# Kernel tuning notes

Hardware: AMD Instinct MI355X
Metric: run time of the kernel (lower is better)

The kernel has to match this reference:

```python
import jax, jax.numpy as jnp
import numpy as np

D_MODEL = 1024
N_HEAD = 16
D_QKV = 64
B, L = 2, 2048
LN_EPS = 1e-5


def setup_inputs() -> dict:
    key = jax.random.key(0)
    ks = jax.random.split(key, 5)
    # xavier-normal-ish scale for [H, d_model, d_qkv] params
    std_in = (2.0 / (D_MODEL + D_QKV)) ** 0.5
    return {
        "x": jax.random.normal(ks[0], (B, L, D_MODEL), jnp.float32),
        "w_q": jax.random.normal(ks[1], (N_HEAD, D_MODEL, D_QKV), jnp.float32) * std_in,
        "w_k": jax.random.normal(ks[2], (N_HEAD, D_MODEL, D_QKV), jnp.float32) * std_in,
        "w_v": jax.random.normal(ks[3], (N_HEAD, D_MODEL, D_QKV), jnp.float32) * std_in,
        "w_o": jax.random.normal(ks[4], (N_HEAD, D_QKV, D_MODEL), jnp.float32) * std_in,
        "ln_gamma": jnp.ones((D_MODEL,), jnp.float32),
        "ln_beta": jnp.zeros((D_MODEL,), jnp.float32),
    }


def reference(x, w_q, w_k, w_v, w_o, ln_gamma, ln_beta):
    # q,k,v: [B, H, L, d_qkv]
    q = jnp.einsum('hmq,blm->bhlq', w_q, x)
    k = jnp.einsum('hmq,blm->bhlq', w_k, x)
    v = jnp.einsum('hmq,blm->bhlq', w_v, x)
    # scores: [B, H, L, L]
    s = jnp.einsum('bhiq,bhjq->bhij', q, k) / (D_QKV ** 0.5)
    s = jax.nn.softmax(s, axis=-1)
    # (dropout disabled: eval-mode reference)
    att = jnp.einsum('bhij,bhjq->bhiq', s, v)          # [B, H, L, d_qkv]
    out = jnp.einsum('bhlq,hqm->blm', att, w_o)        # [B, L, d_model]
    y = x + out                                        # residual
    mu = jnp.mean(y, axis=-1, keepdims=True)
    var = jnp.var(y, axis=-1, keepdims=True)
    return (y - mu) * jax.lax.rsqrt(var + LN_EPS) * ln_gamma + ln_beta
```

## Files before the change

kernel.cpp:

```cpp
#include <hip/hip_runtime.h>
#include <hip/hip_bf16.h>
#include <cstdint>

#define B_      2
#define L_      2048
#define DM_     1024
#define H_      16
#define DQ_     64
#define LN_EPS  1e-5f
#define QSCALE  0.1803368801111204f

typedef unsigned short u16;
typedef unsigned int   u32;
typedef __attribute__((ext_vector_type(8)))  short short8;
typedef __attribute__((ext_vector_type(4)))  unsigned short u16x4;
typedef __attribute__((ext_vector_type(4)))  unsigned int   u32x4;
typedef __attribute__((ext_vector_type(4)))  float f32x4;
typedef __attribute__((ext_vector_type(16))) float f32x16;

__device__ __forceinline__ u16 f2b(float f) {
  __hip_bfloat16 h = __float2bfloat16(f);
  return *reinterpret_cast<u16*>(&h);
}
__device__ __forceinline__ u32 pk2(float lo, float hi) {
  return (u32)f2b(lo) | ((u32)f2b(hi) << 16);
}

__device__ __forceinline__ void gl_lds16(const void* g, void* l) {
  auto gp = reinterpret_cast<const __attribute__((address_space(1))) unsigned int*>(
      reinterpret_cast<uintptr_t>(g));
  auto lp = reinterpret_cast<__attribute__((address_space(3))) unsigned int*>(
      reinterpret_cast<uintptr_t>(l));
  __builtin_amdgcn_global_load_lds(gp, lp, 16, 0, 0);
}

__device__ __forceinline__ void bar() { asm volatile("s_barrier" ::: "memory"); }

__device__ __forceinline__ short8 frag8(const u16* base, int row, int lchunk) {
  return *(const short8*)(base + row * 64 + ((lchunk ^ (row & 7)) << 3));
}

__global__ __launch_bounds__(256) void prep_all(
    const float* __restrict__ x, const float* __restrict__ wq,
    const float* __restrict__ wk, const float* __restrict__ wv,
    const float* __restrict__ wo, u16* __restrict__ xb,
    u16* __restrict__ wt, u16* __restrict__ wot) {
  __shared__ float Ls[64][65];
  const int t = threadIdx.x;
  const int bx = blockIdx.x;
  if (bx < 4096) {
    int i = bx * 256 + t;
    float4 v = ((const float4*)x)[i];
    u16x4 o = { f2b(v.x), f2b(v.y), f2b(v.z), f2b(v.w) };
    *(u16x4*)(xb + (size_t)i * 4) = o;
  } else if (bx < 4096 + 768) {
    int b2 = bx - 4096;
    int mt = b2 & 15, h = (b2 >> 4) & 15, wh = b2 >> 8;
    const float* in = ((wh == 0) ? wq : (wh == 1) ? wk : wv) + (size_t)h * DM_ * DQ_;
    #pragma unroll
    for (int i = 0; i < 16; ++i) {
      int idx = i * 256 + t, r = idx >> 6, c = idx & 63;
      Ls[r][c] = in[(size_t)(mt * 64 + r) * DQ_ + c];
    }
    __syncthreads();
    u16* outb = wt + (size_t)(wh * H_ + h) * DQ_ * DM_;
    #pragma unroll
    for (int i = 0; i < 16; ++i) {
      int idx = i * 256 + t, q = idx >> 6, mm = idx & 63;
      outb[(size_t)q * DM_ + mt * 64 + mm] = f2b(Ls[mm][q]);
    }
  } else {
    int b3 = bx - 4864;
    int mt = b3 & 15, kt = b3 >> 4;
    #pragma unroll
    for (int i = 0; i < 16; ++i) {
      int idx = i * 256 + t, r = idx >> 6, c = idx & 63;
      Ls[r][c] = wo[(size_t)(kt * 64 + r) * DM_ + mt * 64 + c];
    }
    __syncthreads();
    #pragma unroll
    for (int i = 0; i < 16; ++i) {
      int idx = i * 256 + t, mm = idx >> 6, kk = idx & 63;
      wot[(size_t)(mt * 64 + mm) * DM_ + kt * 64 + kk] = f2b(Ls[kk][mm]);
    }
  }
}

__global__ __launch_bounds__(512) void qkv_big(const u16* __restrict__ xb,
    const u16* __restrict__ wt, u16* __restrict__ Q, u16* __restrict__ K,
    u16* __restrict__ Vtg) {
  const int raw = blockIdx.x;
  const int swz = (raw & 7) * 24 + (raw >> 3);
  const int nt = swz >> 4, mt = swz & 15;
  __shared__ __align__(16) u16 SH[65536];
  u16* const A0 = SH;
  u16* const B0 = SH + 16384;
  u16* const A1 = SH + 32768;
  u16* const B1 = SH + 49152;
  const int t = threadIdx.x, w = t >> 6, lane = t & 63;
  const int lx = lane & 15, lq = lane >> 4;
  const int r8 = lane >> 3, lc = (lane & 7) ^ r8;
  const int row0 = mt * 256, n0 = nt * 256;
  const int wr = (w >> 2) * 128, wc = (w & 3) * 64;

  const u16* gA = xb + (size_t)(row0 + w * 32 + r8) * DM_ + lc * 8;
  const u16* gB = wt + (size_t)(n0  + w * 32 + r8) * DM_ + lc * 8;
  const int lw = (w * 32) * 64;

  #pragma unroll
  for (int s = 0; s < 4; ++s)
    gl_lds16(gA + (size_t)s * 8 * DM_, A0 + lw + s * 8 * 64);
  #pragma unroll
  for (int s = 0; s < 4; ++s)
    gl_lds16(gB + (size_t)s * 8 * DM_, B0 + lw + s * 8 * 64);
  gl_lds16(gA + 64 + (size_t)0 * 8 * DM_, A1 + lw + 0 * 8 * 64);
  gl_lds16(gA + 64 + (size_t)1 * 8 * DM_, A1 + lw + 1 * 8 * 64);
  asm volatile("s_waitcnt vmcnt(2)" ::: "memory");
  bar();

  f32x4 z = {0.f, 0.f, 0.f, 0.f};
  f32x4 acc[8][4];
  #pragma unroll
  for (int mf = 0; mf < 8; ++mf)
    #pragma unroll
    for (int nf = 0; nf < 4; ++nf) acc[mf][nf] = z;

  for (int tau = 0; tau < 16; ++tau) {
    const int d = tau & 1;
    u16* Ad = d ? A1 : A0;
    u16* Bd = d ? B1 : B0;
    u16* Ao = d ? A0 : A1;
    u16* Bo = d ? B0 : B1;
    const int t1 = (tau + 1 < 16) ? tau + 1 : 15;

    short8 af[8], bf[4];
    #pragma unroll
    for (int mf = 0; mf < 8; ++mf) af[mf] = frag8(Ad, wr + mf * 16 + lx, lq);
    #pragma unroll
    for (int nf = 0; nf < 4; ++nf) bf[nf] = frag8(Bd, wc + nf * 16 + lx, lq);

    gl_lds16(gA + (size_t)t1 * 64 + (size_t)2 * 8 * DM_, Ao + lw + 2 * 8 * 64);
    gl_lds16(gA + (size_t)t1 * 64 + (size_t)3 * 8 * DM_, Ao + lw + 3 * 8 * 64);
    #pragma unroll
    for (int s = 0; s < 4; ++s)
      gl_lds16(gB + (size_t)t1 * 64 + (size_t)s * 8 * DM_, Bo + lw + s * 8 * 64);

    #pragma unroll
    for (int nf = 0; nf < 4; ++nf)
      #pragma unroll
      for (int mf = 0; mf < 8; ++mf)
        acc[mf][nf] = __builtin_amdgcn_mfma_f32_16x16x32_bf16(af[mf], bf[nf], acc[mf][nf], 0, 0, 0);

    #pragma unroll
    for (int mf = 0; mf < 8; ++mf) af[mf] = frag8(Ad, wr + mf * 16 + lx, 4 | lq);
    #pragma unroll
    for (int nf = 0; nf < 4; ++nf) bf[nf] = frag8(Bd, wc + nf * 16 + lx, 4 | lq);
    #pragma unroll
    for (int nf = 0; nf < 4; ++nf)
      #pragma unroll
      for (int mf = 0; mf < 8; ++mf)
        acc[mf][nf] = __builtin_amdgcn_mfma_f32_16x16x32_bf16(af[mf], bf[nf], acc[mf][nf], 0, 0, 0);

    bar();

    const int t2 = (tau + 2 < 16) ? tau + 2 : 15;
    gl_lds16(gA + (size_t)t2 * 64 + (size_t)0 * 8 * DM_, Ad + lw + 0 * 8 * 64);
    gl_lds16(gA + (size_t)t2 * 64 + (size_t)1 * 8 * DM_, Ad + lw + 1 * 8 * 64);

    asm volatile("s_waitcnt vmcnt(2)" ::: "memory");
    bar();
  }
  asm volatile("s_waitcnt vmcnt(0)" ::: "memory");
  bar();

  const int wh  = nt >> 2;
  const float oscale = (wh == 0) ? QSCALE : 1.0f;
  const int bb  = row0 >> 11, l0 = row0 & 2047;
  const int hd0 = (nt & 3) * 256;
  u16* Ep = SH;

  if (wh != 2) {
    u16* outp = (wh == 0) ? Q : K;
    #pragma unroll
    for (int mp = 0; mp < 2; ++mp) {
      if ((w >> 2) == mp) {
        #pragma unroll
        for (int mf = 0; mf < 8; ++mf)
          #pragma unroll
          for (int nf = 0; nf < 4; ++nf)
            #pragma unroll
            for (int r = 0; r < 4; ++r) {
              int l = mf * 16 + lq * 4 + r;
              Ep[l * 264 + wc + nf * 16 + lx] = f2b(acc[mf][nf][r] * oscale);
            }
      }
      __syncthreads();
      #pragma unroll
      for (int hs = 0; hs < 4; ++hs) {
        const int hh = (hd0 >> 6) + hs;
        u16* gbase = outp + ((size_t)(bb * H_ + hh) * L_ + l0 + mp * 128) * DQ_;
        #pragma unroll
        for (int it = 0; it < 2; ++it) {
          int u = it * 512 + t;
          int l = u >> 3, ch = u & 7;
          *(uint4*)(gbase + (size_t)u * 8) = *(const uint4*)&Ep[l * 264 + hs * 64 + ch * 8];
        }
      }
      __syncthreads();
    }
  } else {
    #pragma unroll
    for (int mp = 0; mp < 2; ++mp) {
      if ((w >> 2) == mp) {
        #pragma unroll
        for (int mf = 0; mf < 8; ++mf)
          #pragma unroll
          for (int nf = 0; nf < 4; ++nf) {
            int ll = mf * 16 + lq * 4;
            int lp = (ll & ~12) | ((ll & 4) << 1) | ((ll & 8) >> 1);
            int dd = wc + nf * 16 + lx;
            uint2 pv = { pk2(acc[mf][nf][0], acc[mf][nf][1]),
                         pk2(acc[mf][nf][2], acc[mf][nf][3]) };
            *(uint2*)&Ep[dd * 136 + lp] = pv;
          }
      }
      __syncthreads();
      #pragma unroll
      for (int it = 0; it < 8; ++it) {
        int v = it * 512 + t;
        int dloc = v >> 4, ch = v & 15;
        int hh = (hd0 + dloc) >> 6, ddg = (hd0 + dloc) & 63;
        u16* g = Vtg + ((size_t)(bb * H_ + hh) * DQ_ + ddg) * L_ + l0 + mp * 128 + ch * 8;
        *(uint4*)g = *(const uint4*)&Ep[dloc * 136 + ch * 8];
      }
      __syncthreads();
    }
  }
}

__global__ __launch_bounds__(512) void attn_mfma(const u16* __restrict__ Q,
    const u16* __restrict__ K, const u16* __restrict__ Vtg, u16* __restrict__ att) {
  const int ord = blockIdx.x;
  const int r_  = ord & 7, s_ = ord >> 3;
  const int qt  = s_ & 7, ghi = s_ >> 3;
  const int grp = r_ + 8 * ghi;
  const int h   = grp & 15, b = grp >> 4;
  __shared__ __align__(16) u16 Qs_[256 * 64];
  __shared__ __align__(16) u16 Ks_[2][64 * 64];
  __shared__ __align__(16) u16 Vt_[2][64 * 64];
  const int t = threadIdx.x, w = t >> 6, lane = t & 63;
  const int c = lane & 31, lsel = lane >> 5;
  const int r8 = lane >> 3, lc = (lane & 7) ^ r8;
  const size_t bh  = (size_t)(b * H_ + h) * L_ * DQ_;
  const size_t bhv = (size_t)(b * H_ + h) * DQ_ * L_;

  const u16* gQ = Q + bh + (size_t)(qt * 256 + w * 32 + r8) * DQ_ + lc * 8;
  #pragma unroll
  for (int i = 0; i < 4; ++i) gl_lds16(gQ + (size_t)i * 8 * DQ_, Qs_ + (w * 32 + i * 8) * 64);

  const u16* gK = K   + bh  + (size_t)(w * 8 + r8) * DQ_ + lc * 8;
  const u16* gV = Vtg + bhv + (size_t)(w * 8 + r8) * L_  + lc * 8;

  gl_lds16(gK, Ks_[0] + w * 8 * 64);
  gl_lds16(gV, Vt_[0] + w * 8 * 64);
  __syncthreads();
  short8 qb[4];
  #pragma unroll
  for (int km = 0; km < 4; ++km) qb[km] = frag8(Qs_, w * 32 + c, (km << 1) | lsel);

  f32x16 zz = {0.f,0.f,0.f,0.f,0.f,0.f,0.f,0.f,0.f,0.f,0.f,0.f,0.f,0.f,0.f,0.f};
  f32x16 oacc0 = zz, oacc1 = zz, lacc = zz;
  const short one_bf = (short)0x3F80;
  short8 ones = {one_bf, one_bf, one_bf, one_bf, one_bf, one_bf, one_bf, one_bf};

  for (int kt = 0; kt < L_ / 64; ++kt) {
    const int cur = kt & 1;
    __syncthreads();

    if (kt + 1 < L_ / 64) {
      const int nxt = 1 - cur;
      gl_lds16(gK + (size_t)(kt + 1) * 64 * DQ_, Ks_[nxt] + w * 8 * 64);
      gl_lds16(gV + (size_t)(kt + 1) * 64,       Vt_[nxt] + w * 8 * 64);
    }

    u32x4 paw[4];
    #pragma unroll
    for (int kb = 0; kb < 2; ++kb) {
      f32x16 s = zz;
      #pragma unroll
      for (int km = 0; km < 4; ++km) {
        short8 ka = frag8(Ks_[cur], kb * 32 + c, (km << 1) | lsel);
        s = __builtin_amdgcn_mfma_f32_32x32x16_bf16(ka, qb[km], s, 0, 0, 0);
      }
      #pragma unroll
      for (int F = 0; F < 2; ++F) {
        u32x4 pw;
        #pragma unroll
        for (int i = 0; i < 4; ++i) {
          float p0 = __builtin_amdgcn_exp2f(s[8 * F + 2 * i]);
          float p1 = __builtin_amdgcn_exp2f(s[8 * F + 2 * i + 1]);
          pw[i] = __builtin_amdgcn_perm(__float_as_uint(p1), __float_as_uint(p0), 0x07060302u);
        }
        paw[2 * kb + F] = pw;
      }
    }

    #pragma unroll
    for (int km = 0; km < 4; ++km) {
      short8 pa  = *reinterpret_cast<const short8*>(&paw[km]);
      short8 vb0 = frag8(Vt_[cur], c,      (km << 1) | lsel);
      short8 vb1 = frag8(Vt_[cur], 32 + c, (km << 1) | lsel);
      oacc0 = __builtin_amdgcn_mfma_f32_32x32x16_bf16(pa, vb0, oacc0, 0, 0, 0);
      oacc1 = __builtin_amdgcn_mfma_f32_32x32x16_bf16(pa, vb1, oacc1, 0, 0, 0);
      lacc  = __builtin_amdgcn_mfma_f32_32x32x16_bf16(pa, ones, lacc, 0, 0, 0);
    }
  }

  const int qrow_base = qt * 256 + w * 32;
  #pragma unroll
  for (int r = 0; r < 16; ++r) {
    int qr = (r & 3) + 8 * (r >> 2) + 4 * lsel;
    float inv = 1.0f / lacc[r];
    size_t base = (size_t)(b * L_ + qrow_base + qr) * DM_ + h * DQ_;
    att[base + c]      = f2b(oacc0[r] * inv);
    att[base + 32 + c] = f2b(oacc1[r] * inv);
  }
}

__global__ __launch_bounds__(256) void oproj_big(const u16* __restrict__ A,
    const u16* __restrict__ wot, float* __restrict__ out) {
  const int nt = blockIdx.x, mt = blockIdx.y;
  __shared__ __align__(16) u16 As_[128 * 64];
  __shared__ __align__(16) u16 Bs_[128 * 64];
  const int t = threadIdx.x, w = t >> 6, lane = t & 63;
  const int lx = lane & 15, lq = lane >> 4;
  const int row0 = mt * 128, n0 = nt * 128;
  const int r8 = lane >> 3, lc = (lane & 7) ^ r8;
  const int wr = (w >> 1) * 64, wc = (w & 1) * 64;

  const u16* gA = A   + (size_t)(row0 + w * 32 + r8) * DM_ + lc * 8;
  const u16* gB = wot + (size_t)(n0  + w * 32 + r8) * DM_ + lc * 8;
  u16* lA = As_ + (w * 32) * 64;
  u16* lB = Bs_ + (w * 32) * 64;

  f32x4 z = {0.f, 0.f, 0.f, 0.f};
  f32x4 acc[4][4];
  #pragma unroll
  for (int mb = 0; mb < 4; ++mb)
    #pragma unroll
    for (int nb = 0; nb < 4; ++nb) acc[mb][nb] = z;

  for (int k0 = 0; k0 < DM_; k0 += 64) {
    #pragma unroll
    for (int i = 0; i < 4; ++i) {
      gl_lds16(gA + (size_t)i * 8 * DM_ + k0, lA + i * 8 * 64);
      gl_lds16(gB + (size_t)i * 8 * DM_ + k0, lB + i * 8 * 64);
    }
    __syncthreads();
    short8 af[4][2];
    #pragma unroll
    for (int mb = 0; mb < 4; ++mb)
      #pragma unroll
      for (int kh = 0; kh < 2; ++kh)
        af[mb][kh] = frag8(As_, wr + mb * 16 + lx, (kh << 2) | lq);
    #pragma unroll
    for (int nb = 0; nb < 4; ++nb) {
      short8 b0 = frag8(Bs_, wc + nb * 16 + lx, lq);
      short8 b1 = frag8(Bs_, wc + nb * 16 + lx, 4 | lq);
      #pragma unroll
      for (int mb = 0; mb < 4; ++mb) {
        acc[mb][nb] = __builtin_amdgcn_mfma_f32_16x16x32_bf16(af[mb][0], b0, acc[mb][nb], 0, 0, 0);
        acc[mb][nb] = __builtin_amdgcn_mfma_f32_16x16x32_bf16(af[mb][1], b1, acc[mb][nb], 0, 0, 0);
      }
    }
    __syncthreads();
  }
  #pragma unroll
  for (int mb = 0; mb < 4; ++mb)
    #pragma unroll
    for (int nb = 0; nb < 4; ++nb)
      #pragma unroll
      for (int r = 0; r < 4; ++r) {
        int row = row0 + wr + mb * 16 + lq * 4 + r;
        out[(size_t)row * DM_ + n0 + wc + nb * 16 + lx] = acc[mb][nb][r];
      }
}

__global__ __launch_bounds__(256) void resid_ln(
    const float* __restrict__ x, const float* __restrict__ gamma,
    const float* __restrict__ beta, float* __restrict__ out) {
  const int row = blockIdx.x;
  const int t   = threadIdx.x;
  const float4* xp = (const float4*)(x   + (size_t)row * DM_);
  float4*       yp = (float4*)      (out + (size_t)row * DM_);

  float4 xv = xp[t];
  float4 av = yp[t];
  float y0 = xv.x + av.x, y1 = xv.y + av.y, y2 = xv.z + av.z, y3 = xv.w + av.w;

  float s  = y0 + y1 + y2 + y3;
  float s2 = y0 * y0 + y1 * y1 + y2 * y2 + y3 * y3;
  #pragma unroll
  for (int off = 32; off > 0; off >>= 1) {
    s  += __shfl_xor(s,  off, 64);
    s2 += __shfl_xor(s2, off, 64);
  }
  __shared__ float red[8];
  const int wave = t >> 6, lane = t & 63;
  if (lane == 0) { red[wave] = s; red[4 + wave] = s2; }
  __syncthreads();
  s  = red[0] + red[1] + red[2] + red[3];
  s2 = red[4] + red[5] + red[6] + red[7];

  const float mean = s * (1.f / DM_);
  const float var  = s2 * (1.f / DM_) - mean * mean;
  const float inv  = rsqrtf(var + LN_EPS);

  const float4 g  = ((const float4*)gamma)[t];
  const float4 bt = ((const float4*)beta)[t];
  float4 r;
  r.x = (y0 - mean) * inv * g.x + bt.x;
  r.y = (y1 - mean) * inv * g.y + bt.y;
  r.z = (y2 - mean) * inv * g.z + bt.z;
  r.w = (y3 - mean) * inv * g.w + bt.w;
  yp[t] = r;
}

extern "C" void kernel_launch(void* const* d_in, const int* in_sizes, int n_in,
                              void* d_out, int out_size, void* d_ws, size_t ws_size,
                              hipStream_t stream) {
  const float* x     = (const float*)d_in[0];
  const float* wq    = (const float*)d_in[1];
  const float* wk    = (const float*)d_in[2];
  const float* wv    = (const float*)d_in[3];
  const float* wo    = (const float*)d_in[4];
  const float* gamma = (const float*)d_in[5];
  const float* beta  = (const float*)d_in[6];
  float* out = (float*)d_out;

  char* ws = (char*)d_ws;
  u16* xb  = (u16*)ws;
  u16* Qb  = (u16*)(ws + ((size_t)8  << 20));
  u16* Kb  = (u16*)(ws + ((size_t)16 << 20));
  u16* Vtg = (u16*)(ws + ((size_t)24 << 20));
  u16* wt  = (u16*)(ws + ((size_t)32 << 20));
  u16* wot = (u16*)(ws + ((size_t)38 << 20));
  u16* att = (u16*)(ws + ((size_t)40 << 20));

  prep_all <<<5120, 256, 0, stream>>>(x, wq, wk, wv, wo, xb, wt, wot);
  qkv_big  <<<192, 512, 0, stream>>>(xb, wt, Qb, Kb, Vtg);
  attn_mfma<<<256, 512, 0, stream>>>(Qb, Kb, Vtg, att);
  oproj_big<<<dim3(8, 32), 256, 0, stream>>>(att, wot, out);
  resid_ln <<<B_ * L_, 256, 0, stream>>>(x, gamma, beta, out);
}
```

Measured before the change: 184.1 us.

## Split attention over two key halves and add a combine kernel

The attention kernel now splits the key/value sequence in two, launching twice as many blocks. Each block writes unnormalized fp32 partial outputs and row sums to workspace. A new attn_combine kernel adds the two partials, normalizes them and writes the bf16 attention output for the output projection. The aim is more blocks in flight per CU to hide latency in the attention loop. The cost is an extra launch and roughly tens of MB of fp32 partial traffic, and the workspace must hold buffers up to about 100 MB.

```diff
diff --git a/kernel.cpp b/kernel.cpp
--- a/kernel.cpp
+++ b/kernel.cpp
@@ -239,10 +239,11 @@
 }
 
 __global__ __launch_bounds__(512) void attn_mfma(const u16* __restrict__ Q,
-    const u16* __restrict__ K, const u16* __restrict__ Vtg, u16* __restrict__ att) {
+    const u16* __restrict__ K, const u16* __restrict__ Vtg,
+    float* __restrict__ Opart, float* __restrict__ lsum) {
   const int ord = blockIdx.x;
   const int r_  = ord & 7, s_ = ord >> 3;
-  const int qt  = s_ & 7, ghi = s_ >> 3;
+  const int qt  = s_ & 7, hf = (s_ >> 3) & 1, ghi = s_ >> 4;
   const int grp = r_ + 8 * ghi;
   const int h   = grp & 15, b = grp >> 4;
   __shared__ __align__(16) u16 Qs_[256 * 64];
@@ -253,13 +254,14 @@
   const int r8 = lane >> 3, lc = (lane & 7) ^ r8;
   const size_t bh  = (size_t)(b * H_ + h) * L_ * DQ_;
   const size_t bhv = (size_t)(b * H_ + h) * DQ_ * L_;
+  const int kb0 = hf * (L_ / 2);
 
   const u16* gQ = Q + bh + (size_t)(qt * 256 + w * 32 + r8) * DQ_ + lc * 8;
   #pragma unroll
   for (int i = 0; i < 4; ++i) gl_lds16(gQ + (size_t)i * 8 * DQ_, Qs_ + (w * 32 + i * 8) * 64);
 
-  const u16* gK = K   + bh  + (size_t)(w * 8 + r8) * DQ_ + lc * 8;
-  const u16* gV = Vtg + bhv + (size_t)(w * 8 + r8) * L_  + lc * 8;
+  const u16* gK = K   + bh  + (size_t)(kb0 + w * 8 + r8) * DQ_ + lc * 8;
+  const u16* gV = Vtg + bhv + (size_t)(w * 8 + r8) * L_ + kb0 + lc * 8;
 
   gl_lds16(gK, Ks_[0] + w * 8 * 64);
   gl_lds16(gV, Vt_[0] + w * 8 * 64);
@@ -273,11 +275,11 @@
   const short one_bf = (short)0x3F80;
   short8 ones = {one_bf, one_bf, one_bf, one_bf, one_bf, one_bf, one_bf, one_bf};
 
-  for (int kt = 0; kt < L_ / 64; ++kt) {
+  for (int kt = 0; kt < 16; ++kt) {
     const int cur = kt & 1;
     __syncthreads();
 
-    if (kt + 1 < L_ / 64) {
+    if (kt + 1 < 16) {
       const int nxt = 1 - cur;
       gl_lds16(gK + (size_t)(kt + 1) * 64 * DQ_, Ks_[nxt] + w * 8 * 64);
       gl_lds16(gV + (size_t)(kt + 1) * 64,       Vt_[nxt] + w * 8 * 64);
@@ -317,14 +319,32 @@
   }
 
   const int qrow_base = qt * 256 + w * 32;
+  float* Op = Opart + ((size_t)((hf * 2 + b) * H_ + h) * L_) * DQ_;
+  float* Ls = lsum  +  (size_t)((hf * 2 + b) * H_ + h) * L_;
   #pragma unroll
   for (int r = 0; r < 16; ++r) {
-    int qr = (r & 3) + 8 * (r >> 2) + 4 * lsel;
-    float inv = 1.0f / lacc[r];
-    size_t base = (size_t)(b * L_ + qrow_base + qr) * DM_ + h * DQ_;
-    att[base + c]      = f2b(oacc0[r] * inv);
-    att[base + 32 + c] = f2b(oacc1[r] * inv);
-  }
+    int qg = qrow_base + (r & 3) + 8 * (r >> 2) + 4 * lsel;
+    Op[(size_t)qg * DQ_ + c]      = oacc0[r];
+    Op[(size_t)qg * DQ_ + 32 + c] = oacc1[r];
+    if (c == 0) Ls[qg] = lacc[r];
+  }
+}
+
+__global__ __launch_bounds__(256) void attn_combine(
+    const float* __restrict__ Opart, const float* __restrict__ lsum,
+    u16* __restrict__ att) {
+  const int row = blockIdx.x;
+  const int b = row >> 11, l = row & 2047;
+  const int t = threadIdx.x;
+  const int h = t >> 4, dd = (t & 15) * 4;
+  const size_t g0 = ((size_t)((0 + b) * H_ + h) * L_ + l);
+  const size_t g1 = ((size_t)((2 + b) * H_ + h) * L_ + l);
+  float4 a  = *(const float4*)(Opart + g0 * DQ_ + dd);
+  float4 c4 = *(const float4*)(Opart + g1 * DQ_ + dd);
+  float inv = 1.0f / (lsum[g0] + lsum[g1]);
+  u16x4 o = { f2b((a.x + c4.x) * inv), f2b((a.y + c4.y) * inv),
+              f2b((a.z + c4.z) * inv), f2b((a.w + c4.w) * inv) };
+  *(u16x4*)(att + (size_t)row * DM_ + h * 64 + dd) = o;
 }
 
 __global__ __launch_bounds__(256) void oproj_big(const u16* __restrict__ A,
@@ -439,17 +459,20 @@
   float* out = (float*)d_out;
 
   char* ws = (char*)d_ws;
-  u16* xb  = (u16*)ws;
-  u16* Qb  = (u16*)(ws + ((size_t)8  << 20));
-  u16* Kb  = (u16*)(ws + ((size_t)16 << 20));
-  u16* Vtg = (u16*)(ws + ((size_t)24 << 20));
-  u16* wt  = (u16*)(ws + ((size_t)32 << 20));
-  u16* wot = (u16*)(ws + ((size_t)38 << 20));
-  u16* att = (u16*)(ws + ((size_t)40 << 20));
-
-  prep_all <<<5120, 256, 0, stream>>>(x, wq, wk, wv, wo, xb, wt, wot);
-  qkv_big  <<<192, 512, 0, stream>>>(xb, wt, Qb, Kb, Vtg);
-  attn_mfma<<<256, 512, 0, stream>>>(Qb, Kb, Vtg, att);
-  oproj_big<<<dim3(8, 32), 256, 0, stream>>>(att, wot, out);
-  resid_ln <<<B_ * L_, 256, 0, stream>>>(x, gamma, beta, out);
-}
+  u16* xb   = (u16*)ws;
+  u16* Qb   = (u16*)(ws + ((size_t)8  << 20));
+  u16* Kb   = (u16*)(ws + ((size_t)16 << 20));
+  u16* Vtg  = (u16*)(ws + ((size_t)24 << 20));
+  u16* wt   = (u16*)(ws + ((size_t)32 << 20));
+  u16* wot  = (u16*)(ws + ((size_t)38 << 20));
+  u16* att  = (u16*)(ws + ((size_t)40 << 20));
+  float* Op = (float*)(ws + ((size_t)64 << 20));
+  float* Ls = (float*)(ws + ((size_t)100 << 20));
+
+  prep_all    <<<5120, 256, 0, stream>>>(x, wq, wk, wv, wo, xb, wt, wot);
+  qkv_big     <<<192, 512, 0, stream>>>(xb, wt, Qb, Kb, Vtg);
+  attn_mfma   <<<512, 512, 0, stream>>>(Qb, Kb, Vtg, Op, Ls);
+  attn_combine<<<B_ * L_, 256, 0, stream>>>(Op, Ls, att);
+  oproj_big   <<<dim3(8, 32), 256, 0, stream>>>(att, wot, out);
+  resid_ln    <<<B_ * L_, 256, 0, stream>>>(x, gamma, beta, out);
+}
```

Measured after the change: 190.2 us. +3.3%, slower.
